# Kernel tuning notes

Hardware: AMD Instinct MI355X
Metric: run time of the kernel (lower is better)

## Reference

```python
import jax, jax.numpy as jnp
import numpy as np

BS, L, D = 32, 512, 512
N_CHARS = 32
DICT = 97

def setup_inputs() -> dict:
    key = jax.random.key(0)
    ks = jax.random.split(key, 10)
    s = 1.0 / np.sqrt(D)
    return {
        "inp": jax.random.normal(ks[0], (BS, L, D), jnp.float32),
        "emb": jax.random.normal(ks[1], (N_CHARS, D), jnp.float32) * 0.02,  # embedding table; char_orders == arange
        "Wo_w": jax.random.normal(ks[2], (D, D), jnp.float32) * s,
        "Wo_b": jnp.zeros((D,), jnp.float32),
        "Wv_w": jax.random.normal(ks[3], (D, D), jnp.float32) * s,
        "Wv_b": jnp.zeros((D,), jnp.float32),
        "We_w": jax.random.normal(ks[4], (D, 1), jnp.float32) * s,
        "We_b": jnp.zeros((1,), jnp.float32),
        "Wc_w": jax.random.normal(ks[5], (D, DICT), jnp.float32) * s,
        "Wc_b": jnp.zeros((DICT,), jnp.float32),
    }

def reference(inp, emb, Wo_w, Wo_b, Wv_w, Wv_b, We_w, We_b, Wc_w, Wc_b):
    # O = embedding(arange(max_n_chars)) is just the full embedding table: (n, d)
    w_o = emb @ Wo_w + Wo_b                      # (n, d)
    w_v = inp @ Wv_w + Wv_b                      # (b, L, d)
    # broadcast add -> tanh -> score projection: (b, n, L, d) -> (b, n, L)
    h = jnp.tanh(w_o[None, :, None, :] + w_v[:, None, :, :])
    e = jnp.einsum('bnld,d->bnl', h, We_w[:, 0]) + We_b[0]
    alpha = jax.nn.softmax(e, axis=2)            # softmax over L (axis=2)
    visual_features = jnp.einsum('bnl,bld->bnd', alpha, inp)  # (b, n, d)
    logits = visual_features @ Wc_w + Wc_b       # (b, n, dict)
    return (visual_features, logits)
```

## Files before the change

### kernel.cpp

```cpp
#include <hip/hip_runtime.h>
#include <hip/hip_bf16.h>

#define BS    32
#define LSEQ  512
#define DIM   512
#define NCH   32
#define NDICT 97
#define CHB   16

#define TANH_SCALE 2.8853900817779268f

typedef __attribute__((ext_vector_type(8))) short bf16x8;
typedef __attribute__((ext_vector_type(4))) float f32x4;

#define GLDS16(gsrc, ldst) \
  __builtin_amdgcn_global_load_lds((const __attribute__((address_space(1))) void*)(gsrc), \
                                   (__attribute__((address_space(3))) void*)(ldst), 16, 0, 0)

__device__ __forceinline__ float sig_from_scaled(float xs) {
    float e2 = __builtin_amdgcn_exp2f(xs);
    return __builtin_amdgcn_rcpf(1.0f + e2);
}

__device__ __forceinline__ void split2u(float x0, float x1, unsigned& hp, unsigned& lp) {
    unsigned r0 = __float_as_uint(x0) + 0x8000u;
    unsigned r1 = __float_as_uint(x1) + 0x8000u;
    float f0 = __uint_as_float(r0 & 0xFFFF0000u);
    float f1 = __uint_as_float(r1 & 0xFFFF0000u);
    hp = (r0 >> 16) | (r1 & 0xFFFF0000u);
    unsigned s0 = __float_as_uint(x0 - f0);
    unsigned s1 = __float_as_uint(x1 - f1);
    lp = (s0 >> 16) | (s1 & 0xFFFF0000u);
}

__global__ __launch_bounds__(256) void k_prep_a(
    const float* __restrict__ in, ushort* __restrict__ hi, ushort* __restrict__ lo)
{
    const int i0 = blockIdx.x * 1024 + threadIdx.x;
    #pragma unroll
    for (int rep = 0; rep < 4; ++rep) {
        const int i = i0 + rep * 256;
        float4 v = ((const float4*)in)[i];
        unsigned h01, l01, h23, l23;
        split2u(v.x, v.y, h01, l01);
        split2u(v.z, v.w, h23, l23);
        ((uint2*)hi)[i] = make_uint2(h01, h23);
        ((uint2*)lo)[i] = make_uint2(l01, l23);
    }
}

__global__ __launch_bounds__(256) void k_misc(
    const float* __restrict__ Wv, ushort* __restrict__ BhiT, ushort* __restrict__ BloT,
    const float* __restrict__ Wo, ushort* __restrict__ WohiT, ushort* __restrict__ WoloT,
    const float* __restrict__ emb, ushort* __restrict__ embH, ushort* __restrict__ embL)
{
    __shared__ float tile[64][65];
    const int bid = blockIdx.x;
    const int t = threadIdx.x;
    if (bid < 128) {
        const bool isWv = bid < 64;
        const float* src = isWv ? Wv : Wo;
        ushort* dH = isWv ? BhiT : WohiT;
        ushort* dL = isWv ? BloT : WoloT;
        const int bb = bid & 63;
        const int k0 = (bb >> 3) * 64, n0 = (bb & 7) * 64;
        const int tr = t >> 4, tc = (t & 15) * 4;
        #pragma unroll
        for (int rr = 0; rr < 64; rr += 16) {
            float4 v = *(const float4*)&src[(size_t)(k0 + rr + tr) * DIM + n0 + tc];
            tile[rr + tr][tc + 0] = v.x; tile[rr + tr][tc + 1] = v.y;
            tile[rr + tr][tc + 2] = v.z; tile[rr + tr][tc + 3] = v.w;
        }
        __syncthreads();
        #pragma unroll
        for (int rr = 0; rr < 64; rr += 16) {
            const int n = rr + tr;
            unsigned h01, l01, h23, l23;
            split2u(tile[tc + 0][n] * TANH_SCALE, tile[tc + 1][n] * TANH_SCALE, h01, l01);
            split2u(tile[tc + 2][n] * TANH_SCALE, tile[tc + 3][n] * TANH_SCALE, h23, l23);
            *(uint2*)&dH[(size_t)(n0 + n) * DIM + k0 + tc] = make_uint2(h01, h23);
            *(uint2*)&dL[(size_t)(n0 + n) * DIM + k0 + tc] = make_uint2(l01, l23);
        }
    } else {
        for (int i = t; i < 4096; i += 256) {
            float4 v = ((const float4*)emb)[i];
            unsigned h01, l01, h23, l23;
            split2u(v.x, v.y, h01, l01);
            split2u(v.z, v.w, h23, l23);
            ((uint2*)embH)[i] = make_uint2(h01, h23);
            ((uint2*)embL)[i] = make_uint2(l01, l23);
        }
    }
}

__global__ __launch_bounds__(256) void k_gemm(
    const ushort* __restrict__ Ahi, const ushort* __restrict__ Alo,
    const ushort* __restrict__ Bhi, const ushort* __restrict__ Blo,
    const float* __restrict__ bias, float* __restrict__ C,
    const ushort* __restrict__ WohiT, const ushort* __restrict__ WoloT,
    const ushort* __restrict__ embH, const ushort* __restrict__ embL,
    const float* __restrict__ Wo_b, float* __restrict__ w_o)
{
    __shared__ ushort AhS[4096], AlS[4096], BhS[4096], BlS[4096];

    const int bid = blockIdx.x;
    const int t = threadIdx.x;
    const int wave = t >> 6, lane = t & 63;

    const int srow = lane >> 2;
    const int sg   = (lane & 3) ^ ((lane >> 3) & 3);

    const int fr   = lane & 15;
    const int fswz = ((lane >> 4) ^ ((fr >> 1) & 3)) * 8;

    if (bid < 512) {
        const int mb = (bid & 7) * 16 + (bid >> 5);
        const int nb = (bid >> 3) & 3;
        const int bm = mb * 128, bn = nb * 128;
        const int wm = wave >> 1, wn = wave & 1;
        const int arow0 = (wm * 64 + fr) * 32;
        const int brow0 = (wn * 64 + fr) * 32;

        f32x4 acc[4][4] = {};

        for (int k0 = 0; k0 < DIM; k0 += 32) {
            #pragma unroll
            for (int c2 = 0; c2 < 2; ++c2) {
                const int c = wave * 2 + c2;
                const size_t ga = (size_t)(bm + c * 16 + srow) * DIM + k0 + sg * 8;
                const size_t gb = (size_t)(bn + c * 16 + srow) * DIM + k0 + sg * 8;
                GLDS16(Ahi + ga, &AhS[c * 512]);
                GLDS16(Alo + ga, &AlS[c * 512]);
                GLDS16(Bhi + gb, &BhS[c * 512]);
                GLDS16(Blo + gb, &BlS[c * 512]);
            }
            __syncthreads();

            bf16x8 ah[4], al[4], bh[4], bl[4];
            #pragma unroll
            for (int i = 0; i < 4; ++i) {
                ah[i] = *(const bf16x8*)&AhS[arow0 + i * 512 + fswz];
                al[i] = *(const bf16x8*)&AlS[arow0 + i * 512 + fswz];
                bh[i] = *(const bf16x8*)&BhS[brow0 + i * 512 + fswz];
                bl[i] = *(const bf16x8*)&BlS[brow0 + i * 512 + fswz];
            }
            #pragma unroll
            for (int i = 0; i < 4; ++i)
                #pragma unroll
                for (int j = 0; j < 4; ++j) {
                    acc[i][j] = __builtin_amdgcn_mfma_f32_16x16x32_bf16(ah[i], bh[j], acc[i][j], 0, 0, 0);
                    acc[i][j] = __builtin_amdgcn_mfma_f32_16x16x32_bf16(ah[i], bl[j], acc[i][j], 0, 0, 0);
                    acc[i][j] = __builtin_amdgcn_mfma_f32_16x16x32_bf16(al[i], bh[j], acc[i][j], 0, 0, 0);
                }
            __syncthreads();
        }

        #pragma unroll
        for (int i = 0; i < 4; ++i) {
            const int m = bm + wm * 64 + i * 16 + (lane >> 4) * 4;
            #pragma unroll
            for (int j = 0; j < 4; ++j) {
                const int n = bn + wn * 64 + j * 16 + fr;
                const float bb = TANH_SCALE * bias[n];
                #pragma unroll
                for (int r = 0; r < 4; ++r)
                    C[(size_t)(m + r) * DIM + n] = acc[i][j][r] + bb;
            }
        }
    } else {
        const int nb0 = (bid - 512) * 128;
        const int crow0 = (wave * 32 + fr) * 32;
        f32x4 acc[2][2] = {};

        for (int k0 = 0; k0 < DIM; k0 += 32) {
            #pragma unroll
            for (int c4 = 0; c4 < 4; ++c4) {
                const int idx = wave * 4 + c4;
                const int pl = idx & 1, c = idx >> 1;
                const size_t gb = (size_t)(nb0 + c * 16 + srow) * DIM + k0 + sg * 8;
                if (pl) { GLDS16(WoloT + gb, &BlS[c * 512]); }
                else    { GLDS16(WohiT + gb, &BhS[c * 512]); }
            }
            bf16x8 eh[2], el[2];
            #pragma unroll
            for (int m = 0; m < 2; ++m) {
                const size_t ra = (size_t)(m * 16 + fr) * DIM + k0 + (lane >> 4) * 8;
                eh[m] = *(const bf16x8*)&embH[ra];
                el[m] = *(const bf16x8*)&embL[ra];
            }
            __syncthreads();

            bf16x8 bh[2], bl[2];
            #pragma unroll
            for (int j = 0; j < 2; ++j) {
                bh[j] = *(const bf16x8*)&BhS[crow0 + j * 512 + fswz];
                bl[j] = *(const bf16x8*)&BlS[crow0 + j * 512 + fswz];
            }
            #pragma unroll
            for (int m = 0; m < 2; ++m)
                #pragma unroll
                for (int j = 0; j < 2; ++j) {
                    acc[m][j] = __builtin_amdgcn_mfma_f32_16x16x32_bf16(eh[m], bh[j], acc[m][j], 0, 0, 0);
                    acc[m][j] = __builtin_amdgcn_mfma_f32_16x16x32_bf16(eh[m], bl[j], acc[m][j], 0, 0, 0);
                    acc[m][j] = __builtin_amdgcn_mfma_f32_16x16x32_bf16(el[m], bh[j], acc[m][j], 0, 0, 0);
                }
            __syncthreads();
        }

        #pragma unroll
        for (int m = 0; m < 2; ++m) {
            const int row = m * 16 + (lane >> 4) * 4;
            #pragma unroll
            for (int j = 0; j < 2; ++j) {
                const int col = nb0 + wave * 32 + j * 16 + fr;
                const float bb = TANH_SCALE * Wo_b[col];
                #pragma unroll
                for (int r = 0; r < 4; ++r)
                    w_o[(size_t)(row + r) * DIM + col] = acc[m][j][r] + bb;
            }
        }
    }
}

__global__ __launch_bounds__(256, 4) void k_e(
    const float* __restrict__ w_v, const float* __restrict__ w_o,
    const float* __restrict__ We_w, float* __restrict__ e)
{
    __shared__ float4 woS[CHB * 128];
    const int lblk = blockIdx.x;
    const int b    = blockIdx.y;
    const int ch0  = blockIdx.z * CHB;
    const int t    = threadIdx.x;

    const float4* wog = ((const float4*)w_o) + ch0 * (DIM / 4);
    #pragma unroll
    for (int i = 0; i < CHB * 128 / 256; ++i)
        woS[t + 256 * i] = wog[t + 256 * i];

    const int wave = t >> 6, lane = t & 63;
    const int g = lane >> 4, j = lane & 15;
    const int l = lblk * 16 + wave * 4 + g;

    const float4* wvp = (const float4*)(w_v + (size_t)(b * LSEQ + l) * DIM);
    const float4* wep = (const float4*)We_w;
    float4 wv[8], we[8];
    #pragma unroll
    for (int k = 0; k < 8; ++k) {
        wv[k] = wvp[16 * k + j];
        we[k] = wep[16 * k + j];
    }
    float wsum = 0.0f;
    #pragma unroll
    for (int k = 0; k < 8; ++k)
        wsum += (we[k].x + we[k].y) + (we[k].z + we[k].w);
    #pragma unroll
    for (int off = 1; off < 16; off <<= 1) wsum += __shfl_xor(wsum, off, 64);

    __syncthreads();

    float sv[CHB];
    #pragma unroll 4
    for (int i = 0; i < CHB; ++i) {
        const float4* wrow = &woS[i * 128];
        float s0 = 0.f, s1 = 0.f, s2 = 0.f, s3 = 0.f;
        #pragma unroll
        for (int k = 0; k < 8; ++k) {
            float4 wo4 = wrow[16 * k + j];
            s0 = fmaf(we[k].x, sig_from_scaled(wo4.x + wv[k].x), s0);
            s1 = fmaf(we[k].y, sig_from_scaled(wo4.y + wv[k].y), s1);
            s2 = fmaf(we[k].z, sig_from_scaled(wo4.z + wv[k].z), s2);
            s3 = fmaf(we[k].w, sig_from_scaled(wo4.w + wv[k].w), s3);
        }
        sv[i] = (s0 + s1) + (s2 + s3);
    }

    float t2[8];
    #pragma unroll
    for (int i = 0; i < 8; ++i) {
        float a = sv[2 * i]     + __shfl_xor(sv[2 * i],     1, 64);
        float c = sv[2 * i + 1] + __shfl_xor(sv[2 * i + 1], 1, 64);
        t2[i] = (j & 1) ? c : a;
    }
    float t4[4];
    #pragma unroll
    for (int i = 0; i < 4; ++i) {
        float a = t2[2 * i]     + __shfl_xor(t2[2 * i],     2, 64);
        float c = t2[2 * i + 1] + __shfl_xor(t2[2 * i + 1], 2, 64);
        t4[i] = (j & 2) ? c : a;
    }
    float t8[2];
    #pragma unroll
    for (int i = 0; i < 2; ++i) {
        float a = t4[2 * i]     + __shfl_xor(t4[2 * i],     4, 64);
        float c = t4[2 * i + 1] + __shfl_xor(t4[2 * i + 1], 4, 64);
        t8[i] = (j & 4) ? c : a;
    }
    float a = t8[0] + __shfl_xor(t8[0], 8, 64);
    float c = t8[1] + __shfl_xor(t8[1], 8, 64);
    float res = (j & 8) ? c : a;

    e[(size_t)(b * NCH + ch0 + j) * LSEQ + l] = fmaf(-2.0f, res, wsum);
}

__global__ __launch_bounds__(256) void k_soft(
    const float* __restrict__ e, ushort* __restrict__ aH, ushort* __restrict__ aL)
{
    const int row = blockIdx.x * 4 + (threadIdx.x >> 6);
    const int lane = threadIdx.x & 63;
    const float4* erow = (const float4*)(e + (size_t)row * LSEQ);
    float4 v0 = erow[2 * lane], v1 = erow[2 * lane + 1];
    float m = fmaxf(fmaxf(fmaxf(v0.x, v0.y), fmaxf(v0.z, v0.w)),
                    fmaxf(fmaxf(v1.x, v1.y), fmaxf(v1.z, v1.w)));
    #pragma unroll
    for (int off = 32; off > 0; off >>= 1) m = fmaxf(m, __shfl_xor(m, off, 64));
    float p[8];
    p[0] = __expf(v0.x - m); p[1] = __expf(v0.y - m);
    p[2] = __expf(v0.z - m); p[3] = __expf(v0.w - m);
    p[4] = __expf(v1.x - m); p[5] = __expf(v1.y - m);
    p[6] = __expf(v1.z - m); p[7] = __expf(v1.w - m);
    float s = ((p[0] + p[1]) + (p[2] + p[3])) + ((p[4] + p[5]) + (p[6] + p[7]));
    #pragma unroll
    for (int off = 32; off > 0; off >>= 1) s += __shfl_xor(s, off, 64);
    const float inv = 1.0f / s;
    unsigned h01, l01, h23, l23, h45, l45, h67, l67;
    split2u(p[0] * inv, p[1] * inv, h01, l01);
    split2u(p[2] * inv, p[3] * inv, h23, l23);
    split2u(p[4] * inv, p[5] * inv, h45, l45);
    split2u(p[6] * inv, p[7] * inv, h67, l67);
    uint2* oh = (uint2*)(aH + (size_t)row * LSEQ);
    uint2* ol = (uint2*)(aL + (size_t)row * LSEQ);
    oh[2 * lane]     = make_uint2(h01, h23);
    oh[2 * lane + 1] = make_uint2(h45, h67);
    ol[2 * lane]     = make_uint2(l01, l23);
    ol[2 * lane + 1] = make_uint2(l45, l67);
}

__global__ __launch_bounds__(256) void k_vf(
    const float* __restrict__ inp,
    const ushort* __restrict__ aH, const ushort* __restrict__ aL,
    float* __restrict__ part)
{
    __shared__ unsigned T[4][16 * 68];
    const int dgrp = blockIdx.x >> 1, ls = blockIdx.x & 1;
    const int b = blockIdx.y;
    const int t = threadIdx.x, wave = t >> 6, lane = t & 63;
    const int d0 = (dgrp * 4 + wave) * 16;
    const int lbase = ls * 256;
    const int c = lane & 15, g = lane >> 4;

    unsigned* Tw = T[wave];
    const ushort* aHb = aH + (size_t)b * NCH * LSEQ;
    const ushort* aLb = aL + (size_t)b * NCH * LSEQ;

    f32x4 acc0 = {}, acc1 = {};

    for (int l0 = 0; l0 < 256; l0 += 64) {
        const float4* src = (const float4*)(inp + ((size_t)(b * LSEQ) + lbase + l0 + lane) * DIM + d0);
        float4 v0 = src[0], v1 = src[1], v2 = src[2], v3 = src[3];
        unsigned ev[16];
        {
            unsigned hp, lp;
            split2u(v0.x, v0.y, hp, lp); ev[0] = (lp << 16) | (hp & 0xFFFFu); ev[1] = (lp & 0xFFFF0000u) | (hp >> 16);
            split2u(v0.z, v0.w, hp, lp); ev[2] = (lp << 16) | (hp & 0xFFFFu); ev[3] = (lp & 0xFFFF0000u) | (hp >> 16);
            split2u(v1.x, v1.y, hp, lp); ev[4] = (lp << 16) | (hp & 0xFFFFu); ev[5] = (lp & 0xFFFF0000u) | (hp >> 16);
            split2u(v1.z, v1.w, hp, lp); ev[6] = (lp << 16) | (hp & 0xFFFFu); ev[7] = (lp & 0xFFFF0000u) | (hp >> 16);
            split2u(v2.x, v2.y, hp, lp); ev[8] = (lp << 16) | (hp & 0xFFFFu); ev[9] = (lp & 0xFFFF0000u) | (hp >> 16);
            split2u(v2.z, v2.w, hp, lp); ev[10] = (lp << 16) | (hp & 0xFFFFu); ev[11] = (lp & 0xFFFF0000u) | (hp >> 16);
            split2u(v3.x, v3.y, hp, lp); ev[12] = (lp << 16) | (hp & 0xFFFFu); ev[13] = (lp & 0xFFFF0000u) | (hp >> 16);
            split2u(v3.z, v3.w, hp, lp); ev[14] = (lp << 16) | (hp & 0xFFFFu); ev[15] = (lp & 0xFFFF0000u) | (hp >> 16);
        }
        #pragma unroll
        for (int i = 0; i < 16; ++i)
            Tw[i * 68 + lane] = ev[i];
        #pragma unroll
        for (int ks = 0; ks < 2; ++ks) {
            const unsigned* bp = &Tw[c * 68 + ks * 32 + g * 8];
            uint4 w0 = *(const uint4*)bp;
            uint4 w1 = *(const uint4*)(bp + 4);
            union { unsigned u[4]; bf16x8 v; } H, L;
            H.u[0] = (w0.x & 0xFFFFu) | (w0.y << 16);
            H.u[1] = (w0.z & 0xFFFFu) | (w0.w << 16);
            H.u[2] = (w1.x & 0xFFFFu) | (w1.y << 16);
            H.u[3] = (w1.z & 0xFFFFu) | (w1.w << 16);
            L.u[0] = (w0.x >> 16) | (w0.y & 0xFFFF0000u);
            L.u[1] = (w0.z >> 16) | (w0.w & 0xFFFF0000u);
            L.u[2] = (w1.x >> 16) | (w1.y & 0xFFFF0000u);
            L.u[3] = (w1.z >> 16) | (w1.w & 0xFFFF0000u);

            const int lfrag = lbase + l0 + ks * 32 + g * 8;
            bf16x8 a0h = *(const bf16x8*)&aHb[(size_t)c * LSEQ + lfrag];
            bf16x8 a0l = *(const bf16x8*)&aLb[(size_t)c * LSEQ + lfrag];
            bf16x8 a1h = *(const bf16x8*)&aHb[(size_t)(16 + c) * LSEQ + lfrag];
            bf16x8 a1l = *(const bf16x8*)&aLb[(size_t)(16 + c) * LSEQ + lfrag];

            acc0 = __builtin_amdgcn_mfma_f32_16x16x32_bf16(a0h, H.v, acc0, 0, 0, 0);
            acc0 = __builtin_amdgcn_mfma_f32_16x16x32_bf16(a0h, L.v, acc0, 0, 0, 0);
            acc0 = __builtin_amdgcn_mfma_f32_16x16x32_bf16(a0l, H.v, acc0, 0, 0, 0);
            acc1 = __builtin_amdgcn_mfma_f32_16x16x32_bf16(a1h, H.v, acc1, 0, 0, 0);
            acc1 = __builtin_amdgcn_mfma_f32_16x16x32_bf16(a1h, L.v, acc1, 0, 0, 0);
            acc1 = __builtin_amdgcn_mfma_f32_16x16x32_bf16(a1l, H.v, acc1, 0, 0, 0);
        }
    }

    const size_t base = (size_t)(ls * BS * NCH + b * NCH) * DIM + d0 + c;
    #pragma unroll
    for (int r = 0; r < 4; ++r) {
        part[base + (size_t)(g * 4 + r) * DIM]        = acc0[r];
        part[base + (size_t)(16 + g * 4 + r) * DIM]   = acc1[r];
    }
}

__global__ __launch_bounds__(256) void k_lg(
    const float* __restrict__ part, const float* __restrict__ Wc_w,
    const float* __restrict__ Wc_b, float* __restrict__ out_vf,
    float* __restrict__ out_logits)
{
    __shared__ float vfS[4][DIM];
    __shared__ float lgS[2][4][NDICT];
    const int r0 = blockIdx.x * 4;
    const int t = threadIdx.x;
    const int wave = t >> 6, lane = t & 63;

    const float2* p0 = (const float2*)(part + (size_t)(r0 + wave) * DIM);
    const float2* p1 = (const float2*)(part + (size_t)(BS * NCH + r0 + wave) * DIM);
    float2* vout = (float2*)(out_vf + (size_t)(r0 + wave) * DIM);
    #pragma unroll
    for (int q = 0; q < 4; ++q) {
        float2 x = p0[lane + 64 * q], y = p1[lane + 64 * q];
        float2 z; z.x = x.x + y.x; z.y = x.y + y.y;
        ((float2*)&vfS[wave][0])[lane + 64 * q] = z;
        vout[lane + 64 * q] = z;
    }
    __syncthreads();

    const int j = t & 127, half = t >> 7;
    if (j < NDICT) {
        const float* wc = Wc_w + (size_t)half * 256 * NDICT + j;
        const float* v0 = &vfS[0][half * 256];
        const float* v1 = &vfS[1][half * 256];
        const float* v2 = &vfS[2][half * 256];
        const float* v3 = &vfS[3][half * 256];
        float a0 = 0.f, a1 = 0.f, a2 = 0.f, a3 = 0.f;
        #pragma unroll 4
        for (int d = 0; d < 256; ++d) {
            float w = wc[(size_t)d * NDICT];
            a0 = fmaf(v0[d], w, a0); a1 = fmaf(v1[d], w, a1);
            a2 = fmaf(v2[d], w, a2); a3 = fmaf(v3[d], w, a3);
        }
        lgS[half][0][j] = a0; lgS[half][1][j] = a1;
        lgS[half][2][j] = a2; lgS[half][3][j] = a3;
    }
    __syncthreads();
    for (int idx = t; idx < 4 * NDICT; idx += 256) {
        const int r = idx / NDICT, jj = idx - r * NDICT;
        out_logits[(size_t)(r0 + r) * NDICT + jj] = Wc_b[jj] + lgS[0][r][jj] + lgS[1][r][jj];
    }
}

extern "C" void kernel_launch(void* const* d_in, const int* in_sizes, int n_in,
                              void* d_out, int out_size, void* d_ws, size_t ws_size,
                              hipStream_t stream)
{
    const float* inp  = (const float*)d_in[0];
    const float* emb  = (const float*)d_in[1];
    const float* Wo_w = (const float*)d_in[2];
    const float* Wo_b = (const float*)d_in[3];
    const float* Wv_w = (const float*)d_in[4];
    const float* Wv_b = (const float*)d_in[5];
    const float* We_w = (const float*)d_in[6];
    const float* Wc_w = (const float*)d_in[8];
    const float* Wc_b = (const float*)d_in[9];

    char* p = (char*)d_ws;
    float*  w_o   = (float*)p;  p += (64 << 10);
    float*  ev    = (float*)p;  p += (size_t)BS * NCH * LSEQ * 4;
    ushort* BhiT  = (ushort*)p; p += (size_t)DIM * DIM * 2;
    ushort* BloT  = (ushort*)p; p += (size_t)DIM * DIM * 2;
    ushort* WohiT = (ushort*)p; p += (size_t)DIM * DIM * 2;
    ushort* WoloT = (ushort*)p; p += (size_t)DIM * DIM * 2;
    ushort* embH  = (ushort*)p; p += (size_t)NCH * DIM * 2;
    ushort* embL  = (ushort*)p; p += (size_t)NCH * DIM * 2;
    ushort* aH    = (ushort*)p; p += (size_t)BS * NCH * LSEQ * 2;
    ushort* aL    = (ushort*)p; p += (size_t)BS * NCH * LSEQ * 2;
    float*  partV = (float*)p;  p += (size_t)2 * BS * NCH * DIM * 4;
    ushort* Ahi   = (ushort*)p; p += (size_t)BS * LSEQ * DIM * 2;
    ushort* Alo   = (ushort*)p; p += (size_t)BS * LSEQ * DIM * 2;
    float*  w_v   = (float*)p;

    float* out_vf = (float*)d_out;
    float* out_lg = out_vf + BS * NCH * DIM;

    k_prep_a<<<dim3(2048), dim3(256), 0, stream>>>(inp, Ahi, Alo);
    k_misc<<<dim3(129), dim3(256), 0, stream>>>(Wv_w, BhiT, BloT, Wo_w, WohiT, WoloT, emb, embH, embL);
    k_gemm<<<dim3(516), dim3(256), 0, stream>>>(Ahi, Alo, BhiT, BloT, Wv_b, w_v,
                                                WohiT, WoloT, embH, embL, Wo_b, w_o);
    k_e<<<dim3(LSEQ / 16, BS, NCH / CHB), dim3(256), 0, stream>>>(w_v, w_o, We_w, ev);
    k_soft<<<dim3(256), dim3(256), 0, stream>>>(ev, aH, aL);
    k_vf<<<dim3(16, BS), dim3(256), 0, stream>>>(inp, aH, aL, partV);
    k_lg<<<dim3(256), dim3(256), 0, stream>>>(partV, Wc_w, Wc_b, out_vf, out_lg);
}
```

Measured before the change: 152.9 us.

## Merge prep kernels, double-buffer GEMM LDS stages, widen k_e blocks

```diff
diff --git a/kernel.cpp b/kernel.cpp
--- a/kernel.cpp
+++ b/kernel.cpp
@@ -33,23 +33,8 @@
     lp = (s0 >> 16) | (s1 & 0xFFFF0000u);
 }
 
-__global__ __launch_bounds__(256) void k_prep_a(
-    const float* __restrict__ in, ushort* __restrict__ hi, ushort* __restrict__ lo)
-{
-    const int i0 = blockIdx.x * 1024 + threadIdx.x;
-    #pragma unroll
-    for (int rep = 0; rep < 4; ++rep) {
-        const int i = i0 + rep * 256;
-        float4 v = ((const float4*)in)[i];
-        unsigned h01, l01, h23, l23;
-        split2u(v.x, v.y, h01, l01);
-        split2u(v.z, v.w, h23, l23);
-        ((uint2*)hi)[i] = make_uint2(h01, h23);
-        ((uint2*)lo)[i] = make_uint2(l01, l23);
-    }
-}
-
-__global__ __launch_bounds__(256) void k_misc(
+__global__ __launch_bounds__(256) void k_prep(
+    const float* __restrict__ in, ushort* __restrict__ Ahi, ushort* __restrict__ Alo,
     const float* __restrict__ Wv, ushort* __restrict__ BhiT, ushort* __restrict__ BloT,
     const float* __restrict__ Wo, ushort* __restrict__ WohiT, ushort* __restrict__ WoloT,
     const float* __restrict__ emb, ushort* __restrict__ embH, ushort* __restrict__ embL)
@@ -57,12 +42,24 @@
     __shared__ float tile[64][65];
     const int bid = blockIdx.x;
     const int t = threadIdx.x;
-    if (bid < 128) {
-        const bool isWv = bid < 64;
+    if (bid < 2048) {
+        const int i0 = bid * 1024 + t;
+        #pragma unroll
+        for (int rep = 0; rep < 4; ++rep) {
+            const int i = i0 + rep * 256;
+            float4 v = ((const float4*)in)[i];
+            unsigned h01, l01, h23, l23;
+            split2u(v.x, v.y, h01, l01);
+            split2u(v.z, v.w, h23, l23);
+            ((uint2*)Ahi)[i] = make_uint2(h01, h23);
+            ((uint2*)Alo)[i] = make_uint2(l01, l23);
+        }
+    } else if (bid < 2176) {
+        const bool isWv = bid < 2112;
         const float* src = isWv ? Wv : Wo;
         ushort* dH = isWv ? BhiT : WohiT;
         ushort* dL = isWv ? BloT : WoloT;
-        const int bb = bid & 63;
+        const int bb = (bid - 2048) & 63;
         const int k0 = (bb >> 3) * 64, n0 = (bb & 7) * 64;
         const int tr = t >> 4, tc = (t & 15) * 4;
         #pragma unroll
@@ -101,7 +98,7 @@
     const ushort* __restrict__ embH, const ushort* __restrict__ embL,
     const float* __restrict__ Wo_b, float* __restrict__ w_o)
 {
-    __shared__ ushort AhS[4096], AlS[4096], BhS[4096], BlS[4096];
+    __shared__ ushort AhS[8192], AlS[8192], BhS[8192], BlS[8192];
 
     const int bid = blockIdx.x;
     const int t = threadIdx.x;
@@ -109,7 +106,6 @@
 
     const int srow = lane >> 2;
     const int sg   = (lane & 3) ^ ((lane >> 3) & 3);
-
     const int fr   = lane & 15;
     const int fswz = ((lane >> 4) ^ ((fr >> 1) & 3)) * 8;
 
@@ -123,26 +119,32 @@
 
         f32x4 acc[4][4] = {};
 
-        for (int k0 = 0; k0 < DIM; k0 += 32) {
+        auto stage = [&](int p, int k0) {
             #pragma unroll
             for (int c2 = 0; c2 < 2; ++c2) {
                 const int c = wave * 2 + c2;
                 const size_t ga = (size_t)(bm + c * 16 + srow) * DIM + k0 + sg * 8;
                 const size_t gb = (size_t)(bn + c * 16 + srow) * DIM + k0 + sg * 8;
-                GLDS16(Ahi + ga, &AhS[c * 512]);
-                GLDS16(Alo + ga, &AlS[c * 512]);
-                GLDS16(Bhi + gb, &BhS[c * 512]);
-                GLDS16(Blo + gb, &BlS[c * 512]);
-            }
-            __syncthreads();
-
+                GLDS16(Ahi + ga, &AhS[p * 4096 + c * 512]);
+                GLDS16(Alo + ga, &AlS[p * 4096 + c * 512]);
+                GLDS16(Bhi + gb, &BhS[p * 4096 + c * 512]);
+                GLDS16(Blo + gb, &BlS[p * 4096 + c * 512]);
+            }
+        };
+
+        stage(0, 0);
+        __syncthreads();
+        int cur = 0;
+        for (int ks = 0; ks < 16; ++ks) {
+            if (ks < 15) stage(cur ^ 1, (ks + 1) * 32);
+            const int co = cur * 4096;
             bf16x8 ah[4], al[4], bh[4], bl[4];
             #pragma unroll
             for (int i = 0; i < 4; ++i) {
-                ah[i] = *(const bf16x8*)&AhS[arow0 + i * 512 + fswz];
-                al[i] = *(const bf16x8*)&AlS[arow0 + i * 512 + fswz];
-                bh[i] = *(const bf16x8*)&BhS[brow0 + i * 512 + fswz];
-                bl[i] = *(const bf16x8*)&BlS[brow0 + i * 512 + fswz];
+                ah[i] = *(const bf16x8*)&AhS[co + arow0 + i * 512 + fswz];
+                al[i] = *(const bf16x8*)&AlS[co + arow0 + i * 512 + fswz];
+                bh[i] = *(const bf16x8*)&BhS[co + brow0 + i * 512 + fswz];
+                bl[i] = *(const bf16x8*)&BlS[co + brow0 + i * 512 + fswz];
             }
             #pragma unroll
             for (int i = 0; i < 4; ++i)
@@ -153,6 +155,7 @@
                     acc[i][j] = __builtin_amdgcn_mfma_f32_16x16x32_bf16(al[i], bh[j], acc[i][j], 0, 0, 0);
                 }
             __syncthreads();
+            cur ^= 1;
         }
 
         #pragma unroll
@@ -222,7 +225,7 @@
     }
 }
 
-__global__ __launch_bounds__(256, 4) void k_e(
+__global__ __launch_bounds__(512, 8) void k_e(
     const float* __restrict__ w_v, const float* __restrict__ w_o,
     const float* __restrict__ We_w, float* __restrict__ e)
 {
@@ -234,12 +237,12 @@
 
     const float4* wog = ((const float4*)w_o) + ch0 * (DIM / 4);
     #pragma unroll
-    for (int i = 0; i < CHB * 128 / 256; ++i)
-        woS[t + 256 * i] = wog[t + 256 * i];
+    for (int i = 0; i < 4; ++i)
+        woS[t + 512 * i] = wog[t + 512 * i];
 
     const int wave = t >> 6, lane = t & 63;
     const int g = lane >> 4, j = lane & 15;
-    const int l = lblk * 16 + wave * 4 + g;
+    const int l = lblk * 32 + wave * 4 + g;
 
     const float4* wvp = (const float4*)(w_v + (size_t)(b * LSEQ + l) * DIM);
     const float4* wep = (const float4*)We_w;
@@ -490,11 +493,11 @@
     float* out_vf = (float*)d_out;
     float* out_lg = out_vf + BS * NCH * DIM;
 
-    k_prep_a<<<dim3(2048), dim3(256), 0, stream>>>(inp, Ahi, Alo);
-    k_misc<<<dim3(129), dim3(256), 0, stream>>>(Wv_w, BhiT, BloT, Wo_w, WohiT, WoloT, emb, embH, embL);
+    k_prep<<<dim3(2177), dim3(256), 0, stream>>>(inp, Ahi, Alo, Wv_w, BhiT, BloT,
+                                                 Wo_w, WohiT, WoloT, emb, embH, embL);
     k_gemm<<<dim3(516), dim3(256), 0, stream>>>(Ahi, Alo, BhiT, BloT, Wv_b, w_v,
                                                 WohiT, WoloT, embH, embL, Wo_b, w_o);
-    k_e<<<dim3(LSEQ / 16, BS, NCH / CHB), dim3(256), 0, stream>>>(w_v, w_o, We_w, ev);
+    k_e<<<dim3(LSEQ / 32, BS, NCH / CHB), dim3(512), 0, stream>>>(w_v, w_o, We_w, ev);
     k_soft<<<dim3(256), dim3(256), 0, stream>>>(ev, aH, aL);
     k_vf<<<dim3(16, BS), dim3(256), 0, stream>>>(inp, aH, aL, partV);
     k_lg<<<dim3(256), dim3(256), 0, stream>>>(partV, Wc_w, Wc_b, out_vf, out_lg);
```

Result: slower. 534.7 us (+249.7%).
